# Kernel tuning notes

Hardware: AMD Instinct MI355X
Metric: run time of the kernel (lower is better)

## Reference

```python
import jax, jax.numpy as jnp
import numpy as np

N_WIRES = 10
N_OPS = 30
C64 = jnp.complex64

# Frozen random circuit (stand-in for tq.RandomLayer(n_ops=30)): deterministic op list.
_rng = np.random.default_rng(42)
OPS = []
for _ in range(N_OPS):
    k = int(_rng.integers(0, 4))
    if k == 3:
        w = _rng.choice(N_WIRES, size=2, replace=False)
        OPS.append(('cnot', int(w[0]), int(w[1])))
    else:
        OPS.append((('rx', 'ry', 'rz')[k], int(_rng.integers(0, N_WIRES)), -1))


def _rx_mat(t):
    c = jnp.cos(t / 2).astype(C64)
    s = jnp.sin(t / 2).astype(C64)
    return jnp.stack([jnp.stack([c, -1j * s]), jnp.stack([-1j * s, c])])


def _ry_mat(t):
    c = jnp.cos(t / 2).astype(C64)
    s = jnp.sin(t / 2).astype(C64)
    return jnp.stack([jnp.stack([c, -s]), jnp.stack([s, c])])


def _rz_mat(t):
    tc = t.astype(C64)
    z = jnp.zeros((), C64)
    return jnp.stack([jnp.stack([jnp.exp(-1j * tc / 2), z]), jnp.stack([z, jnp.exp(1j * tc / 2)])])

_GATE = {'rx': _rx_mat, 'ry': _ry_mat, 'rz': _rz_mat}


def _apply_1q(state, U, w):
    # state: [bsz] + [2]*N_WIRES ; apply 2x2 U on qubit axis w
    s = jnp.moveaxis(state, 1 + w, -1)
    s = jnp.einsum('ij,...j->...i', U, s)
    return jnp.moveaxis(s, -1, 1 + w)


def _apply_cnot(state, c, t):
    s = jnp.moveaxis(state, (1 + c, 1 + t), (-2, -1))
    s = jnp.stack([s[..., 0, :], s[..., 1, ::-1]], axis=-2)  # flip target when control=1
    return jnp.moveaxis(s, (-2, -1), (1 + c, 1 + t))


def _quantum_head(x, rand_params, rx_theta, ry_theta, head_w, head_b):
    bsz = x.shape[0]
    # GeneralEncoder '10xRy': RY(x[:,w])|0> per wire -> product state built directly
    state = jnp.ones((bsz, 1), C64)
    for w in range(N_WIRES):
        vec = jnp.stack([jnp.cos(x[:, w] / 2), jnp.sin(x[:, w] / 2)], axis=-1).astype(C64)
        state = (state[:, :, None] * vec[:, None, :]).reshape(bsz, -1)
    state = state.reshape((bsz,) + (2,) * N_WIRES)
    # RandomLayer (frozen 30-op circuit, one angle per op)
    for i, (kind, a, b) in enumerate(OPS):
        if kind == 'cnot':
            state = _apply_cnot(state, a, b)
        else:
            state = _apply_1q(state, _GATE[kind](rand_params[i]), a)
    # shared trainable RX then RY applied to every wire (single shared param each)
    Urx = _rx_mat(rx_theta[0])
    Ury = _ry_mat(ry_theta[0])
    for w in range(N_WIRES):
        state = _apply_1q(state, Urx, w)
        state = _apply_1q(state, Ury, w)
    # MeasureAll(PauliZ): <Z_w> = P(bit_w=0) - P(bit_w=1)
    probs = jnp.abs(state) ** 2  # float32, [bsz] + [2]*n
    feats = []
    for w in range(N_WIRES):
        axes = tuple(1 + q for q in range(N_WIRES) if q != w)
        p = probs.sum(axis=axes)  # [bsz, 2]
        feats.append(p[:, 0] - p[:, 1])
    feats = jnp.stack(feats, axis=-1)  # [bsz, n_wires]
    return feats @ head_w + head_b[0]


def _mlp(x, w0, b0, w1, b1, w2, b2, w3, b3):
    # faithful to ClassicalMLP: Linear chain with NO activations
    h = x @ w0.T + b0
    h = h @ w1.T + b1
    h = h @ w2.T + b2
    return (h @ w3.T + b3)[:, 0]


def setup_inputs() -> dict:
    key = jax.random.key(0)
    ks = jax.random.split(key, 14)
    BSZ = 8192
    return {
        'state_batch': jax.random.normal(ks[0], (BSZ, N_WIRES), jnp.float32),
        'rand_params': jax.random.normal(ks[1], (N_OPS,), jnp.float32),
        'rx_theta': jax.random.normal(ks[2], (1,), jnp.float32),
        'ry_theta': jax.random.normal(ks[3], (1,), jnp.float32),
        'head_w': jax.random.normal(ks[4], (N_WIRES,), jnp.float32) * 0.3,
        'head_b': jax.random.normal(ks[5], (1,), jnp.float32) * 0.1,
        'w0': jax.random.normal(ks[6], (64, N_WIRES), jnp.float32) * 0.3,
        'b0': jax.random.normal(ks[7], (64,), jnp.float32) * 0.1,
        'w1': jax.random.normal(ks[8], (32, 64), jnp.float32) * 0.12,
        'b1': jax.random.normal(ks[9], (32,), jnp.float32) * 0.1,
        'w2': jax.random.normal(ks[10], (16, 32), jnp.float32) * 0.17,
        'b2': jax.random.normal(ks[11], (16,), jnp.float32) * 0.1,
        'w3': jax.random.normal(ks[12], (1, 16), jnp.float32) * 0.25,
        'b3': jax.random.normal(ks[13], (1,), jnp.float32) * 0.1,
    }


def reference(state_batch, rand_params, rx_theta, ry_theta, head_w, head_b, w0, b0, w1, b1, w2, b2, w3, b3):
    q = _quantum_head(state_batch, rand_params, rx_theta, ry_theta, head_w, head_b)
    c = _mlp(state_batch, w0, b0, w1, b1, w2, b2, w3, b3)
    return q + c
```

## Files before the change

### kernel.cpp

```cpp
#include <hip/hip_runtime.h>
#include <cstdint>

#define NW 10
#define NOPS 30

typedef float v2fp __attribute__((ext_vector_type(2)));

namespace {

typedef unsigned __int128 u128;

struct CRng { u128 state; u128 inc; bool has32; uint32_t cached; };

constexpr u128 PCG_MUL = (((u128)0x2360ED051FC65DA4ULL) << 64) | (u128)0x4385DF649FCCF645ULL;

constexpr void cr_step(CRng &r) { r.state = r.state * PCG_MUL + r.inc; }

constexpr uint64_t cr_out(u128 st) {
  uint64_t hi = (uint64_t)(st >> 64);
  uint64_t lo = (uint64_t)st;
  unsigned rot = (unsigned)(st >> 122) & 63u;
  uint64_t v = hi ^ lo;
  return (v >> rot) | (v << ((64u - rot) & 63u));
}

constexpr uint64_t cr_next64(CRng &r) { cr_step(r); return cr_out(r.state); }

constexpr uint32_t cr_next32(CRng &r) {
  if (r.has32) { r.has32 = false; return r.cached; }
  uint64_t v = cr_next64(r);
  r.has32 = true; r.cached = (uint32_t)(v >> 32);
  return (uint32_t)v;
}

constexpr CRng cr_seed(uint32_t ent) {
  uint32_t pool[4] = {0u, 0u, 0u, 0u};
  uint32_t hc = 0x43b0d7e5u;
  for (int i = 0; i < 4; i++) {
    uint32_t v = (i == 0) ? ent : 0u;
    v ^= hc; hc *= 0x931e8875u; v *= hc; v ^= v >> 16;
    pool[i] = v;
  }
  for (int s = 0; s < 4; s++)
    for (int d = 0; d < 4; d++)
      if (s != d) {
        uint32_t v = pool[s];
        v ^= hc; hc *= 0x931e8875u; v *= hc; v ^= v >> 16;
        uint32_t res = 0xca01f9ddu * pool[d] - 0x4973f715u * v;
        res ^= res >> 16;
        pool[d] = res;
      }
  uint32_t hb = 0x8b51f9ddu;
  uint64_t s64[4] = {0ull, 0ull, 0ull, 0ull};
  for (int i = 0; i < 8; i++) {
    uint32_t d = pool[i & 3];
    d ^= hb; hb *= 0x58f38dedu; d *= hb; d ^= d >> 16;
    if (i & 1) s64[i >> 1] |= ((uint64_t)d << 32); else s64[i >> 1] = (uint64_t)d;
  }
  CRng r{};
  u128 initstate = (((u128)s64[0]) << 64) | (u128)s64[1];
  u128 initseq   = (((u128)s64[2]) << 64) | (u128)s64[3];
  r.state = 0; r.inc = (initseq << 1) | (u128)1;
  cr_step(r);
  r.state += initstate;
  cr_step(r);
  r.has32 = false; r.cached = 0u;
  return r;
}

constexpr uint32_t cr_lemire32(CRng &r, uint32_t rng) {
  uint32_t rng_excl = rng + 1u;
  uint64_t m = (uint64_t)cr_next32(r) * (uint64_t)rng_excl;
  uint32_t leftover = (uint32_t)m;
  if (leftover < rng_excl) {
    uint32_t threshold = (uint32_t)(0xFFFFFFFFu - rng) % rng_excl;
    while (leftover < threshold) {
      m = (uint64_t)cr_next32(r) * (uint64_t)rng_excl;
      leftover = (uint32_t)m;
    }
  }
  return (uint32_t)(m >> 32);
}

constexpr bool canary_pcg42() {
  CRng r = cr_seed(42u);
  double a = (double)(cr_next64(r) >> 11) * (1.0 / 9007199254740992.0);
  double b = (double)(cr_next64(r) >> 11) * (1.0 / 9007199254740992.0);
  double c = (double)(cr_next64(r) >> 11) * (1.0 / 9007199254740992.0);
  bool ok = (a > 0.77395603) && (a < 0.77395607);
  ok = ok && (b > 0.43887842) && (b < 0.43887846);
  ok = ok && (c > 0.85859790) && (c < 0.85859794);
  return ok;
}
static_assert(canary_pcg42(), "CANARY_PCG_SEED42_RANDOM_MISMATCH");

struct COp { int kind; int a; int b; int slot; };
struct Circ { COp op[NOPS]; };

constexpr Circ build_circuit() {
  Circ c{};
  CRng r = cr_seed(42u);
  for (int i = 0; i < NOPS; i++) {
    int k = (int)cr_lemire32(r, 3u);
    if (k == 3) {
      uint32_t v8 = cr_lemire32(r, 8u);
      uint32_t v9 = cr_lemire32(r, 9u);
      uint32_t i0 = v8;
      uint32_t i1 = (v9 == v8) ? 9u : v9;
      uint32_t j = cr_lemire32(r, 1u);
      if (j == 0u) { uint32_t t = i0; i0 = i1; i1 = t; }
      c.op[i] = COp{3, (int)i0, (int)i1, i};
    } else {
      int w = (int)cr_lemire32(r, 9u);
      c.op[i] = COp{k, w, 0, i};
    }
  }
  return c;
}
constexpr Circ CC = build_circuit();

constexpr int MAXP = 16384;
constexpr int MAXU = 4096;

struct Tables {
  int np, nu, overflow;
  uint32_t pmeta[MAXP]; uint32_t pcm[MAXP]; uint32_t psm[MAXP];
  uint32_t upack[MAXU]; int ustart[MAXU + 1];
};

constexpr Tables build_tables() {
  Tables T{};
  uint32_t meta[MAXP] = {}; uint32_t cm[MAXP] = {}; uint32_t sm[MAXP] = {};
  int np = 0; int ovf = 0;
  for (int w = 0; w < NW; w++)
    for (int src = 0; src < 3; src++) {
      uint32_t xm = (src != 0) ? (1u << w) : 0u;
      uint32_t zm = (src != 1) ? (1u << w) : 0u;
      meta[np] = xm | (zm << 10) | ((uint32_t)w << 21) | ((uint32_t)src << 25);
      cm[np] = 0u; sm[np] = 0u; np++;
    }
  for (int k = NOPS - 1; k >= 0 && !ovf; k--) {
    const COp op = CC.op[k];
    if (op.kind == 3) {
      const int c = op.a, t = op.b;
      for (int p = 0; p < np; p++) {
        uint32_t m = meta[p];
        uint32_t xm = m & 1023u, zm = (m >> 10) & 1023u;
        uint32_t xc = (xm >> c) & 1u, zc = (zm >> c) & 1u;
        uint32_t xt = (xm >> t) & 1u, zt = (zm >> t) & 1u;
        uint32_t fl = xc & zt & (1u ^ (xt ^ zc));
        xm ^= xc << t;
        zm ^= zt << c;
        m = (m & ~(1023u | (1023u << 10))) | xm | (zm << 10);
        m ^= fl << 20;
        meta[p] = m;
      }
    } else {
      const int q = op.a, ax = op.kind, bit = op.slot;
      const int n0 = np;
      for (int p = 0; p < n0; p++) {
        uint32_t m = meta[p];
        uint32_t x = (m >> q) & 1u;
        uint32_t z = (m >> (10 + q)) & 1u;
        uint32_t viol = (ax == 0) ? z : (ax == 1) ? (x ^ z) : x;
        if (viol) {
          uint32_t nx = 0, nz = 0, fl = 0;
          if (ax == 0)      { if (x) { nx = 0; nz = 1; fl = 1; } else { nx = 1; nz = 1; fl = 0; } }
          else if (ax == 1) { if (x) { nx = 0; nz = 1; fl = 0; } else { nx = 1; nz = 0; fl = 1; } }
          else              { if (z) { nx = 1; nz = 0; fl = 0; } else { nx = 1; nz = 1; fl = 1; } }
          if (np >= MAXP) { ovf = 1; break; }
          uint32_t m2 = m;
          m2 &= ~((1u << q) | (1u << (10 + q)));
          m2 |= (nx << q) | (nz << (10 + q));
          m2 ^= fl << 20;
          meta[np] = m2; cm[np] = cm[p]; sm[np] = sm[p] | (1u << bit);
          np++;
          cm[p] |= 1u << bit;
        }
      }
    }
  }
  if (ovf) { T.overflow = 1; return T; }
  int n2 = 0;
  for (int p = 0; p < np; p++) {
    uint32_t m = meta[p];
    if ((m & 1023u) & ((m >> 10) & 1023u)) continue;
    meta[n2] = m; cm[n2] = cm[p]; sm[n2] = sm[p]; n2++;
  }
  np = n2;
  int idx[MAXP] = {}; int tmp[MAXP] = {};
  for (int i = 0; i < np; i++) idx[i] = i;
  int hist[1025] = {};
  for (int i = 0; i < 1025; i++) hist[i] = 0;
  for (int i = 0; i < np; i++) hist[1 + (meta[idx[i]] & 1023u)]++;
  for (int i = 0; i < 1024; i++) hist[i + 1] += hist[i];
  for (int i = 0; i < np; i++) tmp[hist[meta[idx[i]] & 1023u]++] = idx[i];
  for (int i = 0; i < 1025; i++) hist[i] = 0;
  for (int i = 0; i < np; i++) hist[1 + ((meta[tmp[i]] >> 10) & 1023u)]++;
  for (int i = 0; i < 1024; i++) hist[i + 1] += hist[i];
  for (int i = 0; i < np; i++) idx[hist[(meta[tmp[i]] >> 10) & 1023u]++] = tmp[i];
  constexpr int P3[5] = {1, 3, 9, 27, 81};
  int nu = 0; uint32_t prev = 0xFFFFFFFFu;
  for (int i = 0; i < np; i++) {
    int p = idx[i];
    uint32_t key = meta[p] & 0xFFFFFu;
    if (key != prev) {
      if (nu >= MAXU) { T.overflow = 2; return T; }
      uint32_t tlo = 0, thi = 0;
      for (int w = 0; w < 5; w++) {
        uint32_t d = ((key >> w) & 1u) ? 1u : (((key >> (10 + w)) & 1u) ? 2u : 0u);
        tlo += d * (uint32_t)P3[w];
      }
      for (int w = 5; w < 10; w++) {
        uint32_t d = ((key >> w) & 1u) ? 1u : (((key >> (10 + w)) & 1u) ? 2u : 0u);
        thi += d * (uint32_t)P3[w - 5];
      }
      T.upack[nu] = tlo | (thi << 8);
      T.ustart[nu] = i; prev = key; nu++;
    }
    T.pmeta[i] = meta[p]; T.pcm[i] = cm[p]; T.psm[i] = sm[p];
  }
  T.ustart[nu] = np;
  T.np = np; T.nu = nu; T.overflow = 0;
  return T;
}

constexpr Tables TT = build_tables();
static_assert(TT.overflow == 0, "PAULI_PATH_OVERFLOW");
static_assert(TT.nu >= 1 && TT.nu <= MAXU, "PAULI_UNIQUE_COUNT_OUT_OF_RANGE");
constexpr int NU = TT.nu;

constexpr int PAIRS_OFF = 16;
constexpr int WOFF = PAIRS_OFF + 2 * NU;

}

__device__ const Tables dTT = TT;

__global__ __launch_bounds__(256) void prep_kernel(
    const float* __restrict__ rand_params,
    const float* __restrict__ rx_theta, const float* __restrict__ ry_theta,
    const float* __restrict__ head_w, const float* __restrict__ head_b,
    const float* __restrict__ w0, const float* __restrict__ b0,
    const float* __restrict__ w1, const float* __restrict__ b1,
    const float* __restrict__ w2, const float* __restrict__ b2,
    const float* __restrict__ w3, const float* __restrict__ b3,
    float* __restrict__ ws)
{
  const int tid = threadIdx.x;
  __shared__ float ct[32], st[32], abr[3], hwsh[10];
  __shared__ float r2[32], r1[64];
  __shared__ int lcnt;

  if (tid == 0) lcnt = 0;
  if (tid < NOPS) {
    float t = rand_params[tid];
    ct[tid] = cosf(t);
    st[tid] = sinf(t);
  }
  if (tid == 30) {
    float tx = rx_theta[0], ty = ry_theta[0];
    abr[0] = cosf(tx) * cosf(ty);
    abr[1] = -sinf(ty);
    abr[2] = sinf(tx) * cosf(ty);
  }
  if (tid < NW) hwsh[tid] = head_w[tid];
  __syncthreads();

  v2fp* pairs = (v2fp*)(ws + PAIRS_OFF);
  for (int u = tid; u < NU; u += 256) {
    float acc = 0.f;
    const int i0 = dTT.ustart[u], i1 = dTT.ustart[u + 1];
    for (int i = i0; i < i1; i++) {
      uint32_t m = dTT.pmeta[i];
      float v = hwsh[(m >> 21) & 15u] * abr[(m >> 25) & 3u];
      if (m & (1u << 20)) v = -v;
      uint32_t c = dTT.pcm[i];
      while (c) { int b = __builtin_ctz(c); v *= ct[b]; c &= c - 1u; }
      uint32_t s = dTT.psm[i];
      while (s) { int b = __builtin_ctz(s); v *= st[b]; s &= s - 1u; }
      acc += v;
    }
    if (fabsf(acc) > 1e-6f) {
      int id = atomicAdd(&lcnt, 1);
      v2fp p;
      p.x = acc;
      p.y = __uint_as_float(dTT.upack[u]);
      pairs[id] = p;
    }
  }
  __syncthreads();
  if (tid == 0) ((int*)ws)[0] = lcnt;

  if (tid < 32) {
    float acc = 0.f;
    for (int k = 0; k < 16; k++) acc += w3[k] * w2[k*32 + tid];
    r2[tid] = acc;
  }
  __syncthreads();
  if (tid < 64) {
    float acc = 0.f;
    for (int k = 0; k < 32; k++) acc += r2[k] * w1[k*64 + tid];
    r1[tid] = acc;
  }
  __syncthreads();
  if (tid < NW) {
    float acc = 0.f;
    for (int k = 0; k < 64; k++) acc += r1[k] * w0[k*NW + tid];
    ws[WOFF + tid] = acc;
  }
  if (tid == NW) {
    float acc = b3[0] + head_b[0];
    for (int k = 0; k < 16; k++) acc += w3[k] * b2[k];
    for (int k = 0; k < 32; k++) acc += r2[k] * b1[k];
    for (int k = 0; k < 64; k++) acc += r1[k] * b0[k];
    ws[WOFF + NW] = acc;
  }
}

__global__ __launch_bounds__(256) void qsim_kernel(
    const float* __restrict__ x,
    const float* __restrict__ ws,
    float* __restrict__ out,
    int bsz)
{
  __shared__ v2fp  Psh[NU];
  __shared__ float Tlo[4][256];
  __shared__ float Thi[4][256];

  const int tid = threadIdx.x;
  const int nu_eff = ((const int*)ws)[0];

  const v2fp* pairs = (const v2fp*)(ws + PAIRS_OFF);
  for (int i = tid; i < nu_eff; i += 256) Psh[i] = pairs[i];
  __syncthreads();

  const int wv = (int)((blockIdx.x * blockDim.x + tid) >> 6);
  const int lane = tid & 63;
  const int e = tid >> 6;
  if (wv >= bsz) return;
  const float* xe = x + wv * NW;

  float cz[NW], sx[NW];
#pragma unroll
  for (int w = 0; w < NW; w++) {
    float xv = xe[w];
    cz[w] = __cosf(xv);
    sx[w] = __sinf(xv);
  }

  for (int t = lane; t < 243; t += 64) {
    float vlo = 1.f, vhi = 1.f;
    int q = t;
#pragma unroll
    for (int w = 0; w < 5; w++) {
      int d = q % 3; q /= 3;
      vlo *= (d == 1) ? sx[w]     : ((d == 2) ? cz[w]     : 1.0f);
      vhi *= (d == 1) ? sx[w + 5] : ((d == 2) ? cz[w + 5] : 1.0f);
    }
    Tlo[e][t] = vlo;
    Thi[e][t] = vhi;
  }

  float acc = 0.f;
  for (int i = lane; i < nu_eff; i += 64) {
    v2fp pr = Psh[i];
    uint32_t pk = __float_as_uint(pr.y);
    acc += pr.x * Tlo[e][pk & 255u] * Thi[e][pk >> 8];
  }

#pragma unroll
  for (int m = 1; m < 64; m <<= 1) acc += __shfl_xor(acc, m);

  if (lane == 0) {
    float cc = ws[WOFF + NW];
#pragma unroll
    for (int w = 0; w < NW; w++) cc += xe[w] * ws[WOFF + w];
    out[wv] = acc + cc;
  }
}

extern "C" void kernel_launch(void* const* d_in, const int* in_sizes, int n_in,
                              void* d_out, int out_size, void* d_ws, size_t ws_size,
                              hipStream_t stream) {
  const float* x   = (const float*)d_in[0];
  const float* rp  = (const float*)d_in[1];
  const float* rxT = (const float*)d_in[2];
  const float* ryT = (const float*)d_in[3];
  const float* hw  = (const float*)d_in[4];
  const float* hb  = (const float*)d_in[5];
  const float* w0  = (const float*)d_in[6];
  const float* b0  = (const float*)d_in[7];
  const float* w1  = (const float*)d_in[8];
  const float* b1  = (const float*)d_in[9];
  const float* w2  = (const float*)d_in[10];
  const float* b2  = (const float*)d_in[11];
  const float* w3  = (const float*)d_in[12];
  const float* b3  = (const float*)d_in[13];
  const int bsz = in_sizes[0] / NW;

  float* ws = (float*)d_ws;

  hipLaunchKernelGGL(prep_kernel, dim3(1), dim3(256), 0, stream,
                     rp, rxT, ryT, hw, hb, w0, b0, w1, b1, w2, b2, w3, b3, ws);

  const int blocks = (bsz + 3) / 4;
  hipLaunchKernelGGL(qsim_kernel, dim3(blocks), dim3(256), 0, stream,
                     x, ws, (float*)d_out, bsz);
}
```

Before: 99.21 us.

## Drop LDS staging of Pauli pairs and use a fixed padded unrolled loop

Measured after the change: 94.66 us. -4.6%, faster.

```diff
diff --git a/kernel.cpp b/kernel.cpp
--- a/kernel.cpp
+++ b/kernel.cpp
@@ -229,9 +229,10 @@
 static_assert(TT.overflow == 0, "PAULI_PATH_OVERFLOW");
 static_assert(TT.nu >= 1 && TT.nu <= MAXU, "PAULI_UNIQUE_COUNT_OUT_OF_RANGE");
 constexpr int NU = TT.nu;
+constexpr int NUPAD = ((NU + 63) / 64) * 64;
 
 constexpr int PAIRS_OFF = 16;
-constexpr int WOFF = PAIRS_OFF + 2 * NU;
+constexpr int WOFF = PAIRS_OFF + 2 * NUPAD;
 
 }
 
@@ -250,9 +251,7 @@
   const int tid = threadIdx.x;
   __shared__ float ct[32], st[32], abr[3], hwsh[10];
   __shared__ float r2[32], r1[64];
-  __shared__ int lcnt;
-
-  if (tid == 0) lcnt = 0;
+
   if (tid < NOPS) {
     float t = rand_params[tid];
     ct[tid] = cosf(t);
@@ -268,29 +267,27 @@
   __syncthreads();
 
   v2fp* pairs = (v2fp*)(ws + PAIRS_OFF);
-  for (int u = tid; u < NU; u += 256) {
-    float acc = 0.f;
-    const int i0 = dTT.ustart[u], i1 = dTT.ustart[u + 1];
-    for (int i = i0; i < i1; i++) {
-      uint32_t m = dTT.pmeta[i];
-      float v = hwsh[(m >> 21) & 15u] * abr[(m >> 25) & 3u];
-      if (m & (1u << 20)) v = -v;
-      uint32_t c = dTT.pcm[i];
-      while (c) { int b = __builtin_ctz(c); v *= ct[b]; c &= c - 1u; }
-      uint32_t s = dTT.psm[i];
-      while (s) { int b = __builtin_ctz(s); v *= st[b]; s &= s - 1u; }
-      acc += v;
-    }
-    if (fabsf(acc) > 1e-6f) {
-      int id = atomicAdd(&lcnt, 1);
-      v2fp p;
-      p.x = acc;
-      p.y = __uint_as_float(dTT.upack[u]);
-      pairs[id] = p;
-    }
-  }
-  __syncthreads();
-  if (tid == 0) ((int*)ws)[0] = lcnt;
+  for (int u = tid; u < NUPAD; u += 256) {
+    if (u < NU) {
+      float acc = 0.f;
+      const int i0 = dTT.ustart[u], i1 = dTT.ustart[u + 1];
+      for (int i = i0; i < i1; i++) {
+        uint32_t m = dTT.pmeta[i];
+        float v = hwsh[(m >> 21) & 15u] * abr[(m >> 25) & 3u];
+        if (m & (1u << 20)) v = -v;
+        uint32_t c = dTT.pcm[i];
+        while (c) { int b = __builtin_ctz(c); v *= ct[b]; c &= c - 1u; }
+        uint32_t s = dTT.psm[i];
+        while (s) { int b = __builtin_ctz(s); v *= st[b]; s &= s - 1u; }
+        acc += v;
+      }
+      v2fp p; p.x = acc; p.y = __uint_as_float(dTT.upack[u]);
+      pairs[u] = p;
+    } else {
+      v2fp p; p.x = 0.f; p.y = __uint_as_float(0u);
+      pairs[u] = p;
+    }
+  }
 
   if (tid < 32) {
     float acc = 0.f;
@@ -324,17 +321,10 @@
     float* __restrict__ out,
     int bsz)
 {
-  __shared__ v2fp  Psh[NU];
   __shared__ float Tlo[4][256];
   __shared__ float Thi[4][256];
 
   const int tid = threadIdx.x;
-  const int nu_eff = ((const int*)ws)[0];
-
-  const v2fp* pairs = (const v2fp*)(ws + PAIRS_OFF);
-  for (int i = tid; i < nu_eff; i += 256) Psh[i] = pairs[i];
-  __syncthreads();
-
   const int wv = (int)((blockIdx.x * blockDim.x + tid) >> 6);
   const int lane = tid & 63;
   const int e = tid >> 6;
@@ -349,24 +339,30 @@
     sx[w] = __sinf(xv);
   }
 
-  for (int t = lane; t < 243; t += 64) {
-    float vlo = 1.f, vhi = 1.f;
-    int q = t;
-#pragma unroll
-    for (int w = 0; w < 5; w++) {
-      int d = q % 3; q /= 3;
-      vlo *= (d == 1) ? sx[w]     : ((d == 2) ? cz[w]     : 1.0f);
-      vhi *= (d == 1) ? sx[w + 5] : ((d == 2) ? cz[w + 5] : 1.0f);
-    }
-    Tlo[e][t] = vlo;
-    Thi[e][t] = vhi;
-  }
-
+#pragma unroll
+  for (int t0 = 0; t0 < 256; t0 += 64) {
+    const int t = t0 + lane;
+    if (t < 243) {
+      float vlo = 1.f, vhi = 1.f;
+      int q = t;
+#pragma unroll
+      for (int w = 0; w < 5; w++) {
+        int d = q % 3; q /= 3;
+        vlo *= (d == 1) ? sx[w]     : ((d == 2) ? cz[w]     : 1.0f);
+        vhi *= (d == 1) ? sx[w + 5] : ((d == 2) ? cz[w + 5] : 1.0f);
+      }
+      Tlo[e][t] = vlo;
+      Thi[e][t] = vhi;
+    }
+  }
+
+  const v2fp* __restrict__ pairs = (const v2fp*)(ws + PAIRS_OFF);
   float acc = 0.f;
-  for (int i = lane; i < nu_eff; i += 64) {
-    v2fp pr = Psh[i];
+#pragma unroll
+  for (int k = 0; k < NUPAD / 64; k++) {
+    v2fp pr = pairs[lane + 64 * k];
     uint32_t pk = __float_as_uint(pr.y);
-    acc += pr.x * Tlo[e][pk & 255u] * Thi[e][pk >> 8];
+    acc = fmaf(pr.x * Tlo[e][pk & 255u], Thi[e][pk >> 8], acc);
   }
 
 #pragma unroll
```
